# Kernel optimization log

Hardware: AMD Instinct MI355X
Metric: run time of the kernel (lower is better)

The kernel has to match this reference:

```python
import jax, jax.numpy as jnp
import numpy as np

N, C, Wd, Hd = 16, 64, 128, 128


def setup_inputs() -> dict:
    key = jax.random.key(0)
    k = jax.random.split(key, 6)
    return {
        "xR": jax.random.normal(k[0], (N, C, Wd, Hd), dtype=jnp.float32),
        "xT": jax.random.normal(k[1], (N, C, Wd, Hd), dtype=jnp.float32),
        "WR": jax.random.normal(k[2], (C, C), dtype=jnp.float32) * 0.05,
        "bR": jax.random.normal(k[3], (C,), dtype=jnp.float32) * 0.05,
        "WT": jax.random.normal(k[4], (C, C), dtype=jnp.float32) * 0.05,
        "bT": jax.random.normal(k[5], (C,), dtype=jnp.float32) * 0.05,
    }


def reference(xR, xT, WR, bR, WT, bT):
    n, c, w, h = xR.shape
    wh = w * h
    # 1x1 convs (weight [out_c, in_c]) + bias
    xRa = jnp.einsum('nchw,dc->ndhw', xR, WR) + bR[None, :, None, None]
    xTa = jnp.einsum('nchw,dc->ndhw', xT, WT) + bT[None, :, None, None]
    # [N, WH, C] views of adjusted features
    r = xRa.transpose(0, 2, 3, 1).reshape(n, wh, c)
    t = xTa.transpose(0, 2, 3, 1).reshape(n, wh, c)
    # channel self-attention: [N, C, C] = r^T @ r (reduce over WH)
    rs = jnp.einsum('npc,npd->ncd', r, r)
    ts = jnp.einsum('npc,npd->ncd', t, t)
    # concat along channel-row axis and softmax over the 2C rows
    att = jax.nn.softmax(jnp.concatenate([rs, ts], axis=1), axis=1)  # [N, 2C, C]
    # original (unadjusted) features concatenated along channels: [N, WH, 2C]
    rO = xR.transpose(0, 2, 3, 1).reshape(n, wh, c)
    tO = xT.transpose(0, 2, 3, 1).reshape(n, wh, c)
    xO = jnp.concatenate([rO, tO], axis=2)
    out = jnp.einsum('npk,nkc->npc', xO, att)  # [N, WH, C]
    return out.reshape(n, w, h, c).transpose(0, 3, 1, 2)
```

## Files before the change

kernel.cpp:

```cpp
#include <hip/hip_runtime.h>
#include <math.h>

#define WH 16384

typedef __attribute__((ext_vector_type(8))) short short8;
typedef __attribute__((ext_vector_type(4))) float f32x4;

__device__ __forceinline__ void atomAddF(float* p, float v) {
    __hip_atomic_fetch_add(p, v, __ATOMIC_RELAXED, __HIP_MEMORY_SCOPE_AGENT);
}
__device__ __forceinline__ unsigned short f2bf(float x) {
    unsigned u = __float_as_uint(x);
    u += 0x7fff + ((u >> 16) & 1);
    return (unsigned short)(u >> 16);
}
__device__ __forceinline__ float bf2f(unsigned short h) {
    return __uint_as_float(((unsigned)h) << 16);
}

__global__ void zero_ws_kernel(float* __restrict__ p, int n) {
    int i = blockIdx.x * 256 + threadIdx.x;
    if (i < n) p[i] = 0.f;
}

__global__ __launch_bounds__(256, 2) void gram_kernel(
    const float* __restrict__ xR, const float* __restrict__ xT,
    float* __restrict__ G, float* __restrict__ sv) {
    __shared__ unsigned short shi[16384];
    __shared__ unsigned short slo[16384];
    const int t = threadIdx.x, w = t >> 6, lane = t & 63;
    const int n = blockIdx.y, inp = blockIdx.z;
    const float* __restrict__ X = (inp ? xT : xR) + (size_t)n * 64 * WH;
    float* __restrict__ Gout = G + (size_t)(inp * 16 + n) * 4096;
    float* __restrict__ Sout = sv + (size_t)(inp * 16 + n) * 64;
    const int pbase = blockIdx.x << 10;

    f32x4 acc0 = {0.f, 0.f, 0.f, 0.f}, acc1 = acc0, acc2 = acc0, acc3 = acc0;
    float srow[16];
#pragma unroll
    for (int i = 0; i < 16; ++i) srow[i] = 0.f;

    const int g2 = lane >> 1, halfo = (lane & 1) << 2;
    const int m15 = lane & 15, q = lane >> 4;
    const int cha = (w << 4) + m15;
    const int ch0 = m15, ch1 = 16 + m15, ch2 = 32 + m15, ch3 = 48 + m15;

    float4 vbuf[16];
#pragma unroll
    for (int i = 0; i < 16; ++i) {
        const int r = (i << 2) + w;
        vbuf[i] = *(const float4*)(X + (size_t)r * WH + pbase + (lane << 2));
    }

    for (int tile = 0; tile < 4; ++tile) {
        __syncthreads();
#pragma unroll
        for (int i = 0; i < 16; ++i) {
            const int r = (i << 2) + w;
            const float4 v = vbuf[i];
            srow[i] += v.x + v.y + v.z + v.w;
            const unsigned short h0 = f2bf(v.x), h1 = f2bf(v.y), h2 = f2bf(v.z), h3 = f2bf(v.w);
            const unsigned short l0 = f2bf(v.x - bf2f(h0)), l1 = f2bf(v.y - bf2f(h1)),
                                 l2 = f2bf(v.z - bf2f(h2)), l3 = f2bf(v.w - bf2f(h3));
            const int a = (r << 8) + ((g2 ^ (r & 31)) << 3) + halfo;
            *(ushort4*)&shi[a] = make_ushort4(h0, h1, h2, h3);
            *(ushort4*)&slo[a] = make_ushort4(l0, l1, l2, l3);
        }
        __syncthreads();
        if (tile < 3) {
            const int p1 = pbase + ((tile + 1) << 8);
#pragma unroll
            for (int i = 0; i < 16; ++i) {
                const int r = (i << 2) + w;
                vbuf[i] = *(const float4*)(X + (size_t)r * WH + p1 + (lane << 2));
            }
        }
#pragma unroll
        for (int kk = 0; kk < 8; ++kk) {
            const int grp = (kk << 2) + q;
            const int offa = (cha << 8) + ((grp ^ (cha & 31)) << 3);
            const int off0 = (ch0 << 8) + ((grp ^ (ch0 & 31)) << 3);
            const int off1 = (ch1 << 8) + ((grp ^ (ch1 & 31)) << 3);
            const int off2 = (ch2 << 8) + ((grp ^ (ch2 & 31)) << 3);
            const int off3 = (ch3 << 8) + ((grp ^ (ch3 & 31)) << 3);
            const short8 ah = *(const short8*)&shi[offa];
            const short8 al = *(const short8*)&slo[offa];
            const short8 bh0 = *(const short8*)&shi[off0], bl0 = *(const short8*)&slo[off0];
            const short8 bh1 = *(const short8*)&shi[off1], bl1 = *(const short8*)&slo[off1];
            const short8 bh2 = *(const short8*)&shi[off2], bl2 = *(const short8*)&slo[off2];
            const short8 bh3 = *(const short8*)&shi[off3], bl3 = *(const short8*)&slo[off3];
            acc0 = __builtin_amdgcn_mfma_f32_16x16x32_bf16(ah, bh0, acc0, 0, 0, 0);
            acc0 = __builtin_amdgcn_mfma_f32_16x16x32_bf16(ah, bl0, acc0, 0, 0, 0);
            acc0 = __builtin_amdgcn_mfma_f32_16x16x32_bf16(al, bh0, acc0, 0, 0, 0);
            acc0 = __builtin_amdgcn_mfma_f32_16x16x32_bf16(al, bl0, acc0, 0, 0, 0);
            acc1 = __builtin_amdgcn_mfma_f32_16x16x32_bf16(ah, bh1, acc1, 0, 0, 0);
            acc1 = __builtin_amdgcn_mfma_f32_16x16x32_bf16(ah, bl1, acc1, 0, 0, 0);
            acc1 = __builtin_amdgcn_mfma_f32_16x16x32_bf16(al, bh1, acc1, 0, 0, 0);
            acc1 = __builtin_amdgcn_mfma_f32_16x16x32_bf16(al, bl1, acc1, 0, 0, 0);
            acc2 = __builtin_amdgcn_mfma_f32_16x16x32_bf16(ah, bh2, acc2, 0, 0, 0);
            acc2 = __builtin_amdgcn_mfma_f32_16x16x32_bf16(ah, bl2, acc2, 0, 0, 0);
            acc2 = __builtin_amdgcn_mfma_f32_16x16x32_bf16(al, bh2, acc2, 0, 0, 0);
            acc2 = __builtin_amdgcn_mfma_f32_16x16x32_bf16(al, bl2, acc2, 0, 0, 0);
            acc3 = __builtin_amdgcn_mfma_f32_16x16x32_bf16(ah, bh3, acc3, 0, 0, 0);
            acc3 = __builtin_amdgcn_mfma_f32_16x16x32_bf16(ah, bl3, acc3, 0, 0, 0);
            acc3 = __builtin_amdgcn_mfma_f32_16x16x32_bf16(al, bh3, acc3, 0, 0, 0);
            acc3 = __builtin_amdgcn_mfma_f32_16x16x32_bf16(al, bl3, acc3, 0, 0, 0);
        }
    }
    const int rb = (w << 4) + (q << 2);
#pragma unroll
    for (int r = 0; r < 4; ++r) {
        atomAddF(&Gout[(rb + r) * 64 + 0 + m15], acc0[r]);
        atomAddF(&Gout[(rb + r) * 64 + 16 + m15], acc1[r]);
        atomAddF(&Gout[(rb + r) * 64 + 32 + m15], acc2[r]);
        atomAddF(&Gout[(rb + r) * 64 + 48 + m15], acc3[r]);
    }
#pragma unroll
    for (int i = 0; i < 16; ++i) {
        float v = srow[i];
        for (int m = 32; m >= 1; m >>= 1) v += __shfl_xor(v, m, 64);
        if (lane == 0) atomAddF(&Sout[(i << 2) + w], v);
    }
}

__global__ __launch_bounds__(256) void logits_softmax_kernel(
    const float* __restrict__ WR, const float* __restrict__ bR,
    const float* __restrict__ WT, const float* __restrict__ bT,
    const float* __restrict__ G, const float* __restrict__ sv,
    unsigned short* __restrict__ attb) {
    __shared__ float ldsW[4096];
    __shared__ float ldsWt[4096];
    __shared__ float ldsG[4096];
    __shared__ float ldsL[8192];
    __shared__ float ldsS[64], ldsU[64], ldsMx[64], ldsInv[64];
    const int t = threadIdx.x, n = blockIdx.x;
    for (int inp = 0; inp < 2; ++inp) {
        const float* __restrict__ W = inp ? WT : WR;
        const float* __restrict__ b = inp ? bT : bR;
        const float* __restrict__ Gn = G + (size_t)(inp * 16 + n) * 4096;
        const float* __restrict__ sn = sv + (size_t)(inp * 16 + n) * 64;
        __syncthreads();
#pragma unroll
        for (int m = 0; m < 16; ++m) {
            const int idx = t + (m << 8);
            const float wv = W[idx];
            ldsW[idx] = wv;
            ldsWt[((idx & 63) << 6) + (idx >> 6)] = wv;
            ldsG[idx] = Gn[idx];
        }
        if (t < 64) ldsS[t] = sn[t];
        __syncthreads();
        if (t < 64) {
            float u = 0.f;
            for (int c = 0; c < 64; ++c) u += ldsW[(t << 6) + c] * ldsS[c];
            ldsU[t] = u;
        }
        const int d = t >> 2, e0 = (t & 3) << 4;
        float a[16];
#pragma unroll
        for (int e = 0; e < 16; ++e) a[e] = 0.f;
        for (int c = 0; c < 64; ++c) {
            const float wv = ldsW[(d << 6) + c];
#pragma unroll
            for (int e = 0; e < 16; ++e) a[e] += wv * ldsG[(c << 6) + e0 + e];
        }
        __syncthreads();
#pragma unroll
        for (int e = 0; e < 16; ++e) ldsG[(d << 6) + e0 + e] = a[e];
        __syncthreads();
        float r[16];
#pragma unroll
        for (int e = 0; e < 16; ++e) r[e] = 0.f;
        for (int c = 0; c < 64; ++c) {
            const float m1 = ldsG[(d << 6) + c];
#pragma unroll
            for (int e = 0; e < 16; ++e) r[e] += m1 * ldsWt[(c << 6) + e0 + e];
        }
        const float ud = ldsU[d], bd = b[d];
#pragma unroll
        for (int e = 0; e < 16; ++e) {
            const int ee = e0 + e;
            ldsL[((inp << 6) + d) * 64 + ee] =
                r[e] + ud * b[ee] + bd * ldsU[ee] + 16384.f * bd * b[ee];
        }
    }
    __syncthreads();
    if (t < 64) {
        float mx = -1e30f;
        for (int k = 0; k < 128; ++k) mx = fmaxf(mx, ldsL[(k << 6) + t]);
        float s = 0.f;
        for (int k = 0; k < 128; ++k) s += __expf(ldsL[(k << 6) + t] - mx);
        ldsMx[t] = mx;
        ldsInv[t] = 1.f / s;
    }
    __syncthreads();
    unsigned short* __restrict__ an = attb + (size_t)n * 8192;
#pragma unroll
    for (int i = 0; i < 32; ++i) {
        const int idx = (i << 8) + t;
        const int k = idx >> 6, c = idx & 63;
        an[(c << 7) + k] = f2bf(__expf(ldsL[idx] - ldsMx[c]) * ldsInv[c]);
    }
}

__global__ __launch_bounds__(256, 2) void outv_kernel(
    const float* __restrict__ xR, const float* __restrict__ xT,
    const unsigned short* __restrict__ attb, float* __restrict__ out) {
    __shared__ unsigned short lxT[32768];
    __shared__ unsigned short lsa[8192];
    const int t = threadIdx.x, w = t >> 6, lane = t & 63;
    const int m15 = lane & 15, q = lane >> 4;
    const int n = blockIdx.y;
    const int p0 = blockIdx.x << 8;
    const float* __restrict__ XR = xR + (size_t)n * 64 * WH + p0 + t;
    const float* __restrict__ XT = xT + (size_t)n * 64 * WH + p0 + t;
    const unsigned short* __restrict__ an = attb + (size_t)n * 8192;

#pragma unroll
    for (int i = 0; i < 8; ++i) {
        const int idx = (i << 10) + (t << 2);
        const ushort4 av = *(const ushort4*)&an[idx];
        const int c = idx >> 7, ke0 = idx & 127;
        const int slot = ke0 >> 3;
        const int wb = (c << 7) + ((slot ^ (c & 15)) << 3) + (ke0 & 7);
        *(ushort4*)&lsa[wb] = av;
    }
    const int pxm = t & 15;
#pragma unroll
    for (int c4 = 0; c4 < 4; ++c4) {
        const float* __restrict__ base = (c4 < 2) ? XR : XT;
        float v[32];
#pragma unroll
        for (int j = 0; j < 32; ++j)
            v[j] = base[(size_t)((c4 & 1) * 32 + j) * WH];
#pragma unroll
        for (int s = 0; s < 4; ++s) {
            short8 pkt;
#pragma unroll
            for (int e = 0; e < 8; ++e) pkt[e] = (short)f2bf(v[(s << 3) + e]);
            const int slot = (c4 << 2) + s;
            *(short8*)&lxT[(t << 7) + ((slot ^ pxm) << 3)] = pkt;
        }
    }
    __syncthreads();

    f32x4 z = {0.f, 0.f, 0.f, 0.f};
    f32x4 a00 = z, a01 = z, a02 = z, a03 = z;
    f32x4 a10 = z, a11 = z, a12 = z, a13 = z;
    f32x4 a20 = z, a21 = z, a22 = z, a23 = z;
    f32x4 a30 = z, a31 = z, a32 = z, a33 = z;
    const int rA0 = (0 * 16 + m15) << 7, rA1 = (1 * 16 + m15) << 7;
    const int rA2 = (2 * 16 + m15) << 7, rA3 = (3 * 16 + m15) << 7;
    const int rB0 = (((w << 2) + 0) * 16 + m15) << 7;
    const int rB1 = (((w << 2) + 1) * 16 + m15) << 7;
    const int rB2 = (((w << 2) + 2) * 16 + m15) << 7;
    const int rB3 = (((w << 2) + 3) * 16 + m15) << 7;
#pragma unroll
    for (int kg = 0; kg < 4; ++kg) {
        const int sx = (((kg << 2) + q) ^ m15) << 3;
        const short8 A0 = *(const short8*)&lsa[rA0 + sx];
        const short8 A1 = *(const short8*)&lsa[rA1 + sx];
        const short8 A2 = *(const short8*)&lsa[rA2 + sx];
        const short8 A3 = *(const short8*)&lsa[rA3 + sx];
        const short8 B0 = *(const short8*)&lxT[rB0 + sx];
        const short8 B1 = *(const short8*)&lxT[rB1 + sx];
        const short8 B2 = *(const short8*)&lxT[rB2 + sx];
        const short8 B3 = *(const short8*)&lxT[rB3 + sx];
        a00 = __builtin_amdgcn_mfma_f32_16x16x32_bf16(A0, B0, a00, 0, 0, 0);
        a01 = __builtin_amdgcn_mfma_f32_16x16x32_bf16(A0, B1, a01, 0, 0, 0);
        a02 = __builtin_amdgcn_mfma_f32_16x16x32_bf16(A0, B2, a02, 0, 0, 0);
        a03 = __builtin_amdgcn_mfma_f32_16x16x32_bf16(A0, B3, a03, 0, 0, 0);
        a10 = __builtin_amdgcn_mfma_f32_16x16x32_bf16(A1, B0, a10, 0, 0, 0);
        a11 = __builtin_amdgcn_mfma_f32_16x16x32_bf16(A1, B1, a11, 0, 0, 0);
        a12 = __builtin_amdgcn_mfma_f32_16x16x32_bf16(A1, B2, a12, 0, 0, 0);
        a13 = __builtin_amdgcn_mfma_f32_16x16x32_bf16(A1, B3, a13, 0, 0, 0);
        a20 = __builtin_amdgcn_mfma_f32_16x16x32_bf16(A2, B0, a20, 0, 0, 0);
        a21 = __builtin_amdgcn_mfma_f32_16x16x32_bf16(A2, B1, a21, 0, 0, 0);
        a22 = __builtin_amdgcn_mfma_f32_16x16x32_bf16(A2, B2, a22, 0, 0, 0);
        a23 = __builtin_amdgcn_mfma_f32_16x16x32_bf16(A2, B3, a23, 0, 0, 0);
        a30 = __builtin_amdgcn_mfma_f32_16x16x32_bf16(A3, B0, a30, 0, 0, 0);
        a31 = __builtin_amdgcn_mfma_f32_16x16x32_bf16(A3, B1, a31, 0, 0, 0);
        a32 = __builtin_amdgcn_mfma_f32_16x16x32_bf16(A3, B2, a32, 0, 0, 0);
        a33 = __builtin_amdgcn_mfma_f32_16x16x32_bf16(A3, B3, a33, 0, 0, 0);
    }
    float* __restrict__ on = out + (size_t)n * 64 * WH + p0;
#define ST(accv, mt, j)                                                          \
    {                                                                            \
        float* bp = on + (size_t)(((mt) << 4) + (q << 2)) * WH +                 \
                    (((w << 2) + (j)) << 4) + m15;                               \
        bp[0] = accv[0];                                                         \
        bp[WH] = accv[1];                                                        \
        bp[2 * WH] = accv[2];                                                    \
        bp[3 * WH] = accv[3];                                                    \
    }
    ST(a00, 0, 0); ST(a01, 0, 1); ST(a02, 0, 2); ST(a03, 0, 3);
    ST(a10, 1, 0); ST(a11, 1, 1); ST(a12, 1, 2); ST(a13, 1, 3);
    ST(a20, 2, 0); ST(a21, 2, 1); ST(a22, 2, 2); ST(a23, 2, 3);
    ST(a30, 3, 0); ST(a31, 3, 1); ST(a32, 3, 2); ST(a33, 3, 3);
#undef ST
}

extern "C" void kernel_launch(void* const* d_in, const int* in_sizes, int n_in,
                              void* d_out, int out_size, void* d_ws, size_t ws_size,
                              hipStream_t stream) {
    const float* xR = (const float*)d_in[0];
    const float* xT = (const float*)d_in[1];
    const float* WR = (const float*)d_in[2];
    const float* bR = (const float*)d_in[3];
    const float* WT = (const float*)d_in[4];
    const float* bT = (const float*)d_in[5];
    float* out = (float*)d_out;

    float* ws = (float*)d_ws;
    float* G = ws;
    float* sv = ws + 131072;
    unsigned short* attb = (unsigned short*)(ws + 133120);

    zero_ws_kernel<<<520, 256, 0, stream>>>(ws, 133120);
    gram_kernel<<<dim3(16, 16, 2), 256, 0, stream>>>(xR, xT, G, sv);
    logits_softmax_kernel<<<16, 256, 0, stream>>>(WR, bR, WT, bT, G, sv, attb);
    outv_kernel<<<dim3(64, 16), 256, 0, stream>>>(xR, xT, attb, out);
}
```

Before: 246.3 us.

## Halve gram tile width to double grid and parallelize softmax reductions

```diff
diff --git a/kernel.cpp b/kernel.cpp
--- a/kernel.cpp
+++ b/kernel.cpp
@@ -23,66 +23,69 @@
     if (i < n) p[i] = 0.f;
 }
 
-__global__ __launch_bounds__(256, 2) void gram_kernel(
+__global__ __launch_bounds__(256, 4) void gram_kernel(
     const float* __restrict__ xR, const float* __restrict__ xT,
     float* __restrict__ G, float* __restrict__ sv) {
-    __shared__ unsigned short shi[16384];
-    __shared__ unsigned short slo[16384];
+    __shared__ unsigned short shi[8192];
+    __shared__ unsigned short slo[8192];
     const int t = threadIdx.x, w = t >> 6, lane = t & 63;
     const int n = blockIdx.y, inp = blockIdx.z;
     const float* __restrict__ X = (inp ? xT : xR) + (size_t)n * 64 * WH;
     float* __restrict__ Gout = G + (size_t)(inp * 16 + n) * 4096;
     float* __restrict__ Sout = sv + (size_t)(inp * 16 + n) * 64;
-    const int pbase = blockIdx.x << 10;
+    const int pbase = blockIdx.x << 9;
 
     f32x4 acc0 = {0.f, 0.f, 0.f, 0.f}, acc1 = acc0, acc2 = acc0, acc3 = acc0;
-    float srow[16];
-#pragma unroll
-    for (int i = 0; i < 16; ++i) srow[i] = 0.f;
-
-    const int g2 = lane >> 1, halfo = (lane & 1) << 2;
+    float srow[8];
+#pragma unroll
+    for (int i = 0; i < 8; ++i) srow[i] = 0.f;
+
     const int m15 = lane & 15, q = lane >> 4;
+    const int rowh = lane >> 5;
+    const int l31 = lane & 31;
+    const int s2 = l31 >> 1;
+    const int qh = (lane & 1) << 2;
     const int cha = (w << 4) + m15;
     const int ch0 = m15, ch1 = 16 + m15, ch2 = 32 + m15, ch3 = 48 + m15;
 
-    float4 vbuf[16];
-#pragma unroll
-    for (int i = 0; i < 16; ++i) {
-        const int r = (i << 2) + w;
-        vbuf[i] = *(const float4*)(X + (size_t)r * WH + pbase + (lane << 2));
+    float4 vbuf[8];
+#pragma unroll
+    for (int i = 0; i < 8; ++i) {
+        const int r = (i << 3) + (w << 1) + rowh;
+        vbuf[i] = *(const float4*)(X + (size_t)r * WH + pbase + (l31 << 2));
     }
 
     for (int tile = 0; tile < 4; ++tile) {
         __syncthreads();
 #pragma unroll
-        for (int i = 0; i < 16; ++i) {
-            const int r = (i << 2) + w;
+        for (int i = 0; i < 8; ++i) {
+            const int r = (i << 3) + (w << 1) + rowh;
             const float4 v = vbuf[i];
             srow[i] += v.x + v.y + v.z + v.w;
             const unsigned short h0 = f2bf(v.x), h1 = f2bf(v.y), h2 = f2bf(v.z), h3 = f2bf(v.w);
             const unsigned short l0 = f2bf(v.x - bf2f(h0)), l1 = f2bf(v.y - bf2f(h1)),
                                  l2 = f2bf(v.z - bf2f(h2)), l3 = f2bf(v.w - bf2f(h3));
-            const int a = (r << 8) + ((g2 ^ (r & 31)) << 3) + halfo;
+            const int a = (r << 7) + ((s2 ^ (r & 15)) << 3) + qh;
             *(ushort4*)&shi[a] = make_ushort4(h0, h1, h2, h3);
             *(ushort4*)&slo[a] = make_ushort4(l0, l1, l2, l3);
         }
         __syncthreads();
         if (tile < 3) {
-            const int p1 = pbase + ((tile + 1) << 8);
-#pragma unroll
-            for (int i = 0; i < 16; ++i) {
-                const int r = (i << 2) + w;
-                vbuf[i] = *(const float4*)(X + (size_t)r * WH + p1 + (lane << 2));
+            const int p1 = pbase + ((tile + 1) << 7);
+#pragma unroll
+            for (int i = 0; i < 8; ++i) {
+                const int r = (i << 3) + (w << 1) + rowh;
+                vbuf[i] = *(const float4*)(X + (size_t)r * WH + p1 + (l31 << 2));
             }
         }
 #pragma unroll
-        for (int kk = 0; kk < 8; ++kk) {
+        for (int kk = 0; kk < 4; ++kk) {
             const int grp = (kk << 2) + q;
-            const int offa = (cha << 8) + ((grp ^ (cha & 31)) << 3);
-            const int off0 = (ch0 << 8) + ((grp ^ (ch0 & 31)) << 3);
-            const int off1 = (ch1 << 8) + ((grp ^ (ch1 & 31)) << 3);
-            const int off2 = (ch2 << 8) + ((grp ^ (ch2 & 31)) << 3);
-            const int off3 = (ch3 << 8) + ((grp ^ (ch3 & 31)) << 3);
+            const int offa = (cha << 7) + ((grp ^ (cha & 15)) << 3);
+            const int off0 = (ch0 << 7) + ((grp ^ (ch0 & 15)) << 3);
+            const int off1 = (ch1 << 7) + ((grp ^ (ch1 & 15)) << 3);
+            const int off2 = (ch2 << 7) + ((grp ^ (ch2 & 15)) << 3);
+            const int off3 = (ch3 << 7) + ((grp ^ (ch3 & 15)) << 3);
             const short8 ah = *(const short8*)&shi[offa];
             const short8 al = *(const short8*)&slo[offa];
             const short8 bh0 = *(const short8*)&shi[off0], bl0 = *(const short8*)&slo[off0];
@@ -116,10 +119,14 @@
         atomAddF(&Gout[(rb + r) * 64 + 48 + m15], acc3[r]);
     }
 #pragma unroll
-    for (int i = 0; i < 16; ++i) {
+    for (int i = 0; i < 8; ++i) {
         float v = srow[i];
-        for (int m = 32; m >= 1; m >>= 1) v += __shfl_xor(v, m, 64);
-        if (lane == 0) atomAddF(&Sout[(i << 2) + w], v);
+        v += __shfl_xor(v, 16, 64);
+        v += __shfl_xor(v, 8, 64);
+        v += __shfl_xor(v, 4, 64);
+        v += __shfl_xor(v, 2, 64);
+        v += __shfl_xor(v, 1, 64);
+        if (l31 == 0) atomAddF(&Sout[(i << 3) + (w << 1) + rowh], v);
     }
 }
 
@@ -133,6 +140,7 @@
     __shared__ float ldsG[4096];
     __shared__ float ldsL[8192];
     __shared__ float ldsS[64], ldsU[64], ldsMx[64], ldsInv[64];
+    __shared__ float ldsP[256];
     const int t = threadIdx.x, n = blockIdx.x;
     for (int inp = 0; inp < 2; ++inp) {
         const float* __restrict__ W = inp ? WT : WR;
@@ -185,21 +193,34 @@
         }
     }
     __syncthreads();
-    if (t < 64) {
+    const int c = t & 63, seg = t >> 6;
+    {
         float mx = -1e30f;
-        for (int k = 0; k < 128; ++k) mx = fmaxf(mx, ldsL[(k << 6) + t]);
+        for (int k = (seg << 5); k < (seg << 5) + 32; ++k)
+            mx = fmaxf(mx, ldsL[(k << 6) + c]);
+        ldsP[(seg << 6) + c] = mx;
+    }
+    __syncthreads();
+    if (t < 64)
+        ldsMx[t] = fmaxf(fmaxf(ldsP[t], ldsP[64 + t]),
+                         fmaxf(ldsP[128 + t], ldsP[192 + t]));
+    __syncthreads();
+    {
         float s = 0.f;
-        for (int k = 0; k < 128; ++k) s += __expf(ldsL[(k << 6) + t] - mx);
-        ldsMx[t] = mx;
-        ldsInv[t] = 1.f / s;
-    }
+        for (int k = (seg << 5); k < (seg << 5) + 32; ++k)
+            s += __expf(ldsL[(k << 6) + c] - ldsMx[c]);
+        ldsP[(seg << 6) + c] = s;
+    }
+    __syncthreads();
+    if (t < 64)
+        ldsInv[t] = 1.f / (ldsP[t] + ldsP[64 + t] + ldsP[128 + t] + ldsP[192 + t]);
     __syncthreads();
     unsigned short* __restrict__ an = attb + (size_t)n * 8192;
 #pragma unroll
     for (int i = 0; i < 32; ++i) {
         const int idx = (i << 8) + t;
-        const int k = idx >> 6, c = idx & 63;
-        an[(c << 7) + k] = f2bf(__expf(ldsL[idx] - ldsMx[c]) * ldsInv[c]);
+        const int k = idx >> 6, cc = idx & 63;
+        an[(cc << 7) + k] = f2bf(__expf(ldsL[idx] - ldsMx[cc]) * ldsInv[cc]);
     }
 }
 
@@ -317,7 +338,7 @@
     unsigned short* attb = (unsigned short*)(ws + 133120);
 
     zero_ws_kernel<<<520, 256, 0, stream>>>(ws, 133120);
-    gram_kernel<<<dim3(16, 16, 2), 256, 0, stream>>>(xR, xT, G, sv);
+    gram_kernel<<<dim3(32, 16, 2), 256, 0, stream>>>(xR, xT, G, sv);
     logits_softmax_kernel<<<16, 256, 0, stream>>>(WR, bR, WT, bT, G, sv, attb);
     outv_kernel<<<dim3(64, 16), 256, 0, stream>>>(xR, xT, attb, out);
 }
```

After: 247.1 us. Within noise of the previous version (+0.3%).

## Rotate per-batch pixel offsets to spread memory channels; parallelize softmax reductions

Applied to the files above, without the earlier changes.

```diff
diff --git a/kernel.cpp b/kernel.cpp
--- a/kernel.cpp
+++ b/kernel.cpp
@@ -33,7 +33,8 @@
     const float* __restrict__ X = (inp ? xT : xR) + (size_t)n * 64 * WH;
     float* __restrict__ Gout = G + (size_t)(inp * 16 + n) * 4096;
     float* __restrict__ Sout = sv + (size_t)(inp * 16 + n) * 64;
-    const int pbase = blockIdx.x << 10;
+    const int rot = ((n * 2897 + inp * 1451) & 4095) << 2;
+    const int pbase = (blockIdx.x << 10) + rot;
 
     f32x4 acc0 = {0.f, 0.f, 0.f, 0.f}, acc1 = acc0, acc2 = acc0, acc3 = acc0;
     float srow[16];
@@ -49,7 +50,8 @@
 #pragma unroll
     for (int i = 0; i < 16; ++i) {
         const int r = (i << 2) + w;
-        vbuf[i] = *(const float4*)(X + (size_t)r * WH + pbase + (lane << 2));
+        const int px = (pbase + (lane << 2)) & 16383;
+        vbuf[i] = *(const float4*)(X + (size_t)r * WH + px);
     }
 
     for (int tile = 0; tile < 4; ++tile) {
@@ -72,7 +74,8 @@
 #pragma unroll
             for (int i = 0; i < 16; ++i) {
                 const int r = (i << 2) + w;
-                vbuf[i] = *(const float4*)(X + (size_t)r * WH + p1 + (lane << 2));
+                const int px = (p1 + (lane << 2)) & 16383;
+                vbuf[i] = *(const float4*)(X + (size_t)r * WH + px);
             }
         }
 #pragma unroll
@@ -133,6 +136,7 @@
     __shared__ float ldsG[4096];
     __shared__ float ldsL[8192];
     __shared__ float ldsS[64], ldsU[64], ldsMx[64], ldsInv[64];
+    __shared__ float ldsP[256];
     const int t = threadIdx.x, n = blockIdx.x;
     for (int inp = 0; inp < 2; ++inp) {
         const float* __restrict__ W = inp ? WT : WR;
@@ -185,21 +189,34 @@
         }
     }
     __syncthreads();
-    if (t < 64) {
+    const int c = t & 63, seg = t >> 6;
+    {
         float mx = -1e30f;
-        for (int k = 0; k < 128; ++k) mx = fmaxf(mx, ldsL[(k << 6) + t]);
+        for (int k = (seg << 5); k < (seg << 5) + 32; ++k)
+            mx = fmaxf(mx, ldsL[(k << 6) + c]);
+        ldsP[(seg << 6) + c] = mx;
+    }
+    __syncthreads();
+    if (t < 64)
+        ldsMx[t] = fmaxf(fmaxf(ldsP[t], ldsP[64 + t]),
+                         fmaxf(ldsP[128 + t], ldsP[192 + t]));
+    __syncthreads();
+    {
         float s = 0.f;
-        for (int k = 0; k < 128; ++k) s += __expf(ldsL[(k << 6) + t] - mx);
-        ldsMx[t] = mx;
-        ldsInv[t] = 1.f / s;
-    }
+        for (int k = (seg << 5); k < (seg << 5) + 32; ++k)
+            s += __expf(ldsL[(k << 6) + c] - ldsMx[c]);
+        ldsP[(seg << 6) + c] = s;
+    }
+    __syncthreads();
+    if (t < 64)
+        ldsInv[t] = 1.f / (ldsP[t] + ldsP[64 + t] + ldsP[128 + t] + ldsP[192 + t]);
     __syncthreads();
     unsigned short* __restrict__ an = attb + (size_t)n * 8192;
 #pragma unroll
     for (int i = 0; i < 32; ++i) {
         const int idx = (i << 8) + t;
-        const int k = idx >> 6, c = idx & 63;
-        an[(c << 7) + k] = f2bf(__expf(ldsL[idx] - ldsMx[c]) * ldsInv[c]);
+        const int k = idx >> 6, cc = idx & 63;
+        an[(cc << 7) + k] = f2bf(__expf(ldsL[idx] - ldsMx[cc]) * ldsInv[cc]);
     }
 }
 
@@ -211,9 +228,10 @@
     const int t = threadIdx.x, w = t >> 6, lane = t & 63;
     const int m15 = lane & 15, q = lane >> 4;
     const int n = blockIdx.y;
-    const int p0 = blockIdx.x << 8;
-    const float* __restrict__ XR = xR + (size_t)n * 64 * WH + p0 + t;
-    const float* __restrict__ XT = xT + (size_t)n * 64 * WH + p0 + t;
+    const int rotO = ((n * 3217) & 4095) << 2;
+    const int pR = (blockIdx.x << 8) + rotO;
+    const float* __restrict__ XRb = xR + (size_t)n * 64 * WH;
+    const float* __restrict__ XTb = xT + (size_t)n * 64 * WH;
     const unsigned short* __restrict__ an = attb + (size_t)n * 8192;
 
 #pragma unroll
@@ -226,13 +244,14 @@
         *(ushort4*)&lsa[wb] = av;
     }
     const int pxm = t & 15;
+    const int pxt = (pR + t) & 16383;
 #pragma unroll
     for (int c4 = 0; c4 < 4; ++c4) {
-        const float* __restrict__ base = (c4 < 2) ? XR : XT;
+        const float* __restrict__ base = (c4 < 2) ? XRb : XTb;
         float v[32];
 #pragma unroll
         for (int j = 0; j < 32; ++j)
-            v[j] = base[(size_t)((c4 & 1) * 32 + j) * WH];
+            v[j] = base[(size_t)((c4 & 1) * 32 + j) * WH + pxt];
 #pragma unroll
         for (int s = 0; s < 4; ++s) {
             short8 pkt;
@@ -283,11 +302,12 @@
         a32 = __builtin_amdgcn_mfma_f32_16x16x32_bf16(A3, B2, a32, 0, 0, 0);
         a33 = __builtin_amdgcn_mfma_f32_16x16x32_bf16(A3, B3, a33, 0, 0, 0);
     }
-    float* __restrict__ on = out + (size_t)n * 64 * WH + p0;
+    float* __restrict__ on = out + (size_t)n * 64 * WH;
 #define ST(accv, mt, j)                                                          \
     {                                                                            \
-        float* bp = on + (size_t)(((mt) << 4) + (q << 2)) * WH +                 \
-                    (((w << 2) + (j)) << 4) + m15;                               \
+        const int pxl = (((w << 2) + (j)) << 4) + m15;                           \
+        const int pxg = (pR + pxl) & 16383;                                      \
+        float* bp = on + (size_t)(((mt) << 4) + (q << 2)) * WH + pxg;            \
         bp[0] = accv[0];                                                         \
         bp[WH] = accv[1];                                                        \
         bp[2 * WH] = accv[2];                                                    \
```

Measured after the change: 248.2 us. About the same (+0.8%).
